# Performance work log

Hardware: AMD Instinct MI355X
Metric: run time of the kernel (lower is better)

Reference implementation:

```python
import jax, jax.numpy as jnp
import numpy as np

S, H, E, DFF = 8192, 1024, 8, 4096
CAPACITY = (S * 1) // E  # capacity_factor=1.0, k=1 -> 1024 (>= min_capacity 4)


def setup_inputs() -> dict:
    key = jax.random.key(0)
    ks = jax.random.split(key, 6)
    sc_in = 1.0 / np.sqrt(H)
    sc_ff = 1.0 / np.sqrt(DFF)
    return {
        "hidden_states": jax.random.normal(ks[0], (S, H), dtype=jnp.float32),
        "wg": jax.random.normal(ks[1], (H, E), dtype=jnp.float32) * sc_in,
        "w1": jax.random.normal(ks[2], (E, H, DFF), dtype=jnp.float32) * sc_in,
        "b1": jnp.zeros((E, DFF), dtype=jnp.float32),
        "w2": jax.random.normal(ks[3], (E, DFF, H), dtype=jnp.float32) * sc_ff,
        "b2": jnp.zeros((E, H), dtype=jnp.float32),
    }


def _top1_gate(x, wg):
    # DeepSpeed top1gating (noisy_gate_policy=None, used_token=None)
    logits = x @ wg                                   # [S, E]
    gates = jax.nn.softmax(logits, axis=-1)           # [S, E]
    idx = jnp.argmax(gates, axis=-1)                  # [S]
    mask1 = jax.nn.one_hot(idx, E, dtype=gates.dtype) # [S, E]
    # load-balancing aux loss (uses pre-capacity mask)
    me = jnp.mean(gates, axis=0)
    ce = jnp.mean(mask1, axis=0)
    l_aux = jnp.sum(me * ce) * E
    # capacity-based token dropping
    locations1 = jnp.cumsum(mask1, axis=0) - 1.0      # position within expert
    mask1 = mask1 * (locations1 < CAPACITY)
    exp_counts = jnp.sum(mask1, axis=0).astype(jnp.int32)
    loc_s = jnp.sum(locations1 * mask1, axis=1).astype(jnp.int32)   # [S]
    loc_sc = jax.nn.one_hot(loc_s, CAPACITY, dtype=gates.dtype)     # [S, C]
    combine = jnp.einsum("se,sc->sec", gates * mask1, loc_sc)       # [S, E, C]
    dispatch = (combine > 0).astype(gates.dtype)
    return l_aux, combine, dispatch, exp_counts


def reference(hidden_states, wg, w1, b1, w2, b2):
    l_aux, combine, dispatch, exp_counts = _top1_gate(hidden_states, wg)
    # dispatch tokens to expert slots: [E, C, H]
    disp = jnp.einsum("sec,sh->ech", dispatch, hidden_states)
    # grouped expert FFN (GELU MLP)
    h1 = jax.nn.gelu(jnp.einsum("ech,ehf->ecf", disp, w1) + b1[:, None, :])
    eo = jnp.einsum("ecf,efh->ech", h1, w2) + b2[:, None, :]
    # combine back to token order, weighted by gate values
    out = jnp.einsum("sec,ech->sh", combine, eo)      # [S, H]
    # dropout prob = 0.0 -> identity
    return out, l_aux, exp_counts
```

## Files before the change

### kernel.cpp

```cpp
#include <hip/hip_runtime.h>

#define S_TOK 8192
#define H_DIM 1024
#define NE    8
#define CAP   1024
#define DFF   4096

typedef unsigned short u16;
typedef __bf16 bf16_t;
typedef bf16_t bf16x8 __attribute__((ext_vector_type(8)));
typedef float  f32x4  __attribute__((ext_vector_type(4)));
typedef unsigned short u16x8 __attribute__((ext_vector_type(8)));

__device__ __forceinline__ u16 f2bf(float f) {
  union { float f; unsigned u; } a; a.f = f;
  unsigned u = a.u;
  u += 0x7fffu + ((u >> 16) & 1u);
  return (u16)(u >> 16);
}

__device__ __forceinline__ float gelu_fast(float x) {
  float u = 1.5957691216057308f * x * (1.0f + 0.044715f * x * x);
  float ez = __expf(-u);
  return x * __builtin_amdgcn_rcpf(1.0f + ez);
}

__global__ __launch_bounds__(256) void gate_kernel(const float* __restrict__ x,
                                                   const float* __restrict__ wg,
                            float* __restrict__ gate, int* __restrict__ expert,
                            int* __restrict__ rank, int* __restrict__ blockCnt,
                            float* __restrict__ blockMe) {
  __shared__ float sg[16][8];
  __shared__ int   se[16];
  int tid = threadIdx.x, lane = tid & 63, w = tid >> 6;
  int b = blockIdx.x;
  int t0 = w * 4;
  const float* xr[4];
#pragma unroll
  for (int t = 0; t < 4; ++t) xr[t] = x + (size_t)(b * 16 + t0 + t) * H_DIM;

  float acc[4][8];
#pragma unroll
  for (int t = 0; t < 4; ++t)
#pragma unroll
    for (int e = 0; e < 8; ++e) acc[t][e] = 0.f;

#pragma unroll
  for (int i = 0; i < 4; ++i) {
    int h = lane * 4 + i * 256;
    float4 xv[4];
#pragma unroll
    for (int t = 0; t < 4; ++t) xv[t] = *(const float4*)(xr[t] + h);
    float4 wrow[8];
#pragma unroll
    for (int k = 0; k < 4; ++k) {
      wrow[2 * k]     = *(const float4*)(wg + (size_t)(h + k) * 8);
      wrow[2 * k + 1] = *(const float4*)(wg + (size_t)(h + k) * 8 + 4);
    }
#pragma unroll
    for (int t = 0; t < 4; ++t) {
      float xs[4] = {xv[t].x, xv[t].y, xv[t].z, xv[t].w};
#pragma unroll
      for (int k = 0; k < 4; ++k) {
        float xx = xs[k];
        float4 wa = wrow[2 * k], wb = wrow[2 * k + 1];
        acc[t][0] += xx * wa.x; acc[t][1] += xx * wa.y;
        acc[t][2] += xx * wa.z; acc[t][3] += xx * wa.w;
        acc[t][4] += xx * wb.x; acc[t][5] += xx * wb.y;
        acc[t][6] += xx * wb.z; acc[t][7] += xx * wb.w;
      }
    }
  }
#pragma unroll
  for (int off = 32; off >= 1; off >>= 1)
#pragma unroll
    for (int t = 0; t < 4; ++t)
#pragma unroll
      for (int e = 0; e < 8; ++e) acc[t][e] += __shfl_down(acc[t][e], off);

  if (lane == 0) {
#pragma unroll
    for (int t = 0; t < 4; ++t) {
      int tt = t0 + t, s = b * 16 + tt;
      float mx = acc[t][0];
#pragma unroll
      for (int e = 1; e < 8; ++e) mx = fmaxf(mx, acc[t][e]);
      float g[8], Z = 0.f;
#pragma unroll
      for (int e = 0; e < 8; ++e) { g[e] = __expf(acc[t][e] - mx); Z += g[e]; }
      int am = 0; float best = acc[t][0];
#pragma unroll
      for (int e = 1; e < 8; ++e) if (acc[t][e] > best) { best = acc[t][e]; am = e; }
      float inv = 1.f / Z;
#pragma unroll
      for (int e = 0; e < 8; ++e) sg[tt][e] = g[e] * inv;
      se[tt] = am;
      gate[s] = g[am] * inv;
      expert[s] = am;
    }
  }
  __syncthreads();
  if (tid < 16) {
    int e = se[tid], r = 0;
    for (int t2 = 0; t2 < tid; ++t2) r += (se[t2] == e) ? 1 : 0;
    rank[b * 16 + tid] = r;
  }
  if (tid < 8) {
    int c = 0; float m = 0.f;
#pragma unroll
    for (int t = 0; t < 16; ++t) { c += (se[t] == tid) ? 1 : 0; m += sg[t][tid]; }
    blockCnt[b * 8 + tid] = c;
    blockMe[b * 8 + tid] = m;
  }
}

__global__ void scan_kernel(const int* __restrict__ blockCnt, const float* __restrict__ blockMe,
                            int* __restrict__ blockOff, int* __restrict__ counts,
                            float* __restrict__ tail) {
  int tid = threadIdx.x;
  int e = tid >> 6, lane = tid & 63;
  int run = 0; float msum = 0.f;
  for (int c = 0; c < 8; ++c) {
    int b = c * 64 + lane;
    int v = blockCnt[b * 8 + e];
    float mv = blockMe[b * 8 + e];
    int sc = v;
#pragma unroll
    for (int off = 1; off < 64; off <<= 1) {
      int u = __shfl_up(sc, off);
      if (lane >= off) sc += u;
    }
    blockOff[b * 8 + e] = run + sc - v;
    run += __shfl(sc, 63);
#pragma unroll
    for (int off = 32; off >= 1; off >>= 1) mv += __shfl_down(mv, off);
    msum += __shfl(mv, 0);
  }
  __shared__ float sm[8];
  __shared__ int scnt[8];
  if (lane == 0) {
    sm[e] = msum; scnt[e] = run;
    counts[e] = run < CAP ? run : CAP;
  }
  __syncthreads();
  if (tid == 0) {
    float la = 0.f;
    for (int i = 0; i < 8; ++i)
      la += (sm[i] / (float)S_TOK) * ((float)scnt[i] / (float)S_TOK);
    tail[0] = la * (float)NE;
    for (int i = 0; i < 8; ++i) {
      int cc = scnt[i] < CAP ? scnt[i] : CAP;
      tail[1 + i] = (float)cc;
    }
  }
}

__global__ void assign_kernel(const int* __restrict__ expert, const int* __restrict__ rank,
                              const int* __restrict__ blockOff, int* __restrict__ slot_token) {
  int s = blockIdx.x * 256 + threadIdx.x;
  int e = expert[s];
  int pos = blockOff[(s >> 4) * 8 + e] + rank[s];
  if (pos < CAP) slot_token[e * CAP + pos] = s;
}

__global__ void gather_kernel(const float* __restrict__ x, const int* __restrict__ slot_token,
                              const int* __restrict__ counts, u16* __restrict__ disp) {
  int slot = blockIdx.x;
  int e = slot >> 10, c = slot & 1023;
  int t = threadIdx.x;
  ushort4 v4;
  if (c < counts[e]) {
    int s = slot_token[slot];
    float4 v = *(const float4*)(x + (size_t)s * H_DIM + t * 4);
    v4.x = f2bf(v.x); v4.y = f2bf(v.y); v4.z = f2bf(v.z); v4.w = f2bf(v.w);
  } else {
    v4.x = 0; v4.y = 0; v4.z = 0; v4.w = 0;
  }
  *(ushort4*)(disp + (size_t)slot * H_DIM + t * 4) = v4;
}

__global__ void transpose_convert(const float* __restrict__ src0, u16* __restrict__ dst0,
                                  int R, int C) {
  __shared__ float tile[64][65];
  int e = blockIdx.z;
  const float* src = src0 + (size_t)e * R * C;
  u16* dst = dst0 + (size_t)e * R * C;
  int c0 = blockIdx.x * 64, r0 = blockIdx.y * 64;
  int g = threadIdx.x & 15, rr = threadIdx.x >> 4;
#pragma unroll
  for (int p = 0; p < 4; ++p) {
    int r = rr + p * 16;
    float4 v = *(const float4*)(src + (size_t)(r0 + r) * C + c0 + g * 4);
    tile[r][g * 4 + 0] = v.x;
    tile[r][g * 4 + 1] = v.y;
    tile[r][g * 4 + 2] = v.z;
    tile[r][g * 4 + 3] = v.w;
  }
  __syncthreads();
  int g2 = threadIdx.x & 7, c2 = threadIdx.x >> 3;
#pragma unroll
  for (int p = 0; p < 2; ++p) {
    int c = c2 + p * 32;
    u16x8 o;
#pragma unroll
    for (int k = 0; k < 8; ++k) o[k] = f2bf(tile[g2 * 8 + k][c]);
    *(u16x8*)(dst + (size_t)(c0 + c) * R + r0 + g2 * 8) = o;
  }
}

__global__ __launch_bounds__(256, 3) void gemm1_kernel(const u16* __restrict__ disp,
                                                       const u16* __restrict__ w1t,
                                                       const float* __restrict__ b1,
                                                       u16* __restrict__ h1) {
  __shared__ __align__(16) u16 As[8192];
  __shared__ __align__(16) u16 Bs[8192];
  int flat = blockIdx.x;
  int swz = (flat & 7) * 256 + (flat >> 3);
  int e  = swz >> 8;
  int r  = swz & 255;
  int bx = r >> 3;
  int by = r & 7;
  int m0 = by * 128, n0 = bx * 128;
  const u16* A  = disp + (size_t)e * CAP * H_DIM + (size_t)m0 * H_DIM;
  const u16* Bt = w1t + (size_t)e * DFF * H_DIM + (size_t)n0 * H_DIM;

  int tid = threadIdx.x, lane = tid & 63, w = tid >> 6;
  int wm = w >> 1, wn = w & 1, q = lane >> 4, l15 = lane & 15;

  const u16* gpA[4]; const u16* gpB[4]; int lofs[4];
#pragma unroll
  for (int i = 0; i < 4; ++i) {
    int p = (w * 4 + i) * 64 + lane;
    int row = p >> 3, slot = p & 7;
    int kq = slot ^ (row & 7);
    gpA[i] = A + (size_t)row * H_DIM + kq * 8;
    gpB[i] = Bt + (size_t)row * H_DIM + kq * 8;
    lofs[i] = (w * 4 + i) * 512;
  }

  int aoff[2][4], boff[2][4];
#pragma unroll
  for (int t = 0; t < 4; ++t) {
    int ra = wm * 64 + t * 16 + l15;
    int rb = wn * 64 + t * 16 + l15;
#pragma unroll
    for (int s = 0; s < 2; ++s) {
      aoff[s][t] = ra * 64 + (((s * 4) + q) ^ (ra & 7)) * 8;
      boff[s][t] = rb * 64 + (((s * 4) + q) ^ (rb & 7)) * 8;
    }
  }

  f32x4 acc[4][4];
  f32x4 zero = {0.f, 0.f, 0.f, 0.f};
#pragma unroll
  for (int i = 0; i < 4; ++i)
#pragma unroll
    for (int j = 0; j < 4; ++j) acc[i][j] = zero;

  for (int kt = 0; kt < H_DIM; kt += 64) {
#pragma unroll
    for (int i = 0; i < 4; ++i) {
      __builtin_amdgcn_global_load_lds((__attribute__((address_space(1))) int*)(gpA[i] + kt),
                                       (__attribute__((address_space(3))) int*)(As + lofs[i]), 16, 0, 0);
      __builtin_amdgcn_global_load_lds((__attribute__((address_space(1))) int*)(gpB[i] + kt),
                                       (__attribute__((address_space(3))) int*)(Bs + lofs[i]), 16, 0, 0);
    }
    __syncthreads();
#pragma unroll
    for (int s = 0; s < 2; ++s) {
      bf16x8 af[4], bfr[4];
#pragma unroll
      for (int t = 0; t < 4; ++t) af[t] = *(const bf16x8*)(As + aoff[s][t]);
#pragma unroll
      for (int t = 0; t < 4; ++t) bfr[t] = *(const bf16x8*)(Bs + boff[s][t]);
#pragma unroll
      for (int mt = 0; mt < 4; ++mt)
#pragma unroll
        for (int nt = 0; nt < 4; ++nt)
          acc[mt][nt] = __builtin_amdgcn_mfma_f32_16x16x32_bf16(af[mt], bfr[nt], acc[mt][nt], 0, 0, 0);
    }
    __syncthreads();
  }

  const float* b1e = b1 + e * DFF;
  u16* out = h1 + (size_t)e * CAP * DFF;
#pragma unroll
  for (int mt = 0; mt < 4; ++mt)
#pragma unroll
    for (int nt = 0; nt < 4; ++nt) {
      int col = n0 + wn * 64 + nt * 16 + l15;
      float bias = b1e[col];
#pragma unroll
      for (int rr = 0; rr < 4; ++rr) {
        int row = m0 + wm * 64 + mt * 16 + q * 4 + rr;
        out[(size_t)row * DFF + col] = f2bf(gelu_fast(acc[mt][nt][rr] + bias));
      }
    }
}

__global__ __launch_bounds__(512, 4) void gemm2_kernel(const u16* __restrict__ h1,
                                                       const u16* __restrict__ w2t,
                                                       const float* __restrict__ b2,
                                                       const int* __restrict__ slot_token,
                                                       const float* __restrict__ gate,
                                                       const int* __restrict__ counts,
                                                       float* __restrict__ out) {
  __shared__ __align__(16) u16 As[8192];
  __shared__ __align__(16) u16 Bs[8192];
  int flat = blockIdx.x;
  int swz = (flat & 7) * 64 + (flat >> 3);
  int e  = swz >> 6;
  int r  = swz & 63;
  int bx = r & 7;
  int by = r >> 3;
  int m0 = by * 128, n0 = bx * 128;
  const u16* A  = h1 + (size_t)e * CAP * DFF + (size_t)m0 * DFF;
  const u16* Bt = w2t + (size_t)e * H_DIM * DFF + (size_t)n0 * DFF;
  int tid = threadIdx.x, lane = tid & 63, w = tid >> 6;
  int wm = w >> 2, wn = w & 3;
  int q = lane >> 4, l15 = lane & 15;
  f32x4 acc[4][2];
  f32x4 zero = {0.f, 0.f, 0.f, 0.f};
#pragma unroll
  for (int i = 0; i < 4; ++i) { acc[i][0] = zero; acc[i][1] = zero; }

  const u16* gsrc = (w < 4) ? A : Bt;
  u16* ldst = (w < 4) ? As : Bs;
  int q4 = w & 3;
  const u16* gp[4]; int lofs[4];
#pragma unroll
  for (int i = 0; i < 4; ++i) {
    int p = (q4 * 4 + i) * 64 + lane;
    int row = p >> 3, slot = p & 7;
    int kq = slot ^ (row & 7);
    gp[i] = gsrc + (size_t)row * DFF + kq * 8;
    lofs[i] = (q4 * 4 + i) * 512;
  }

  int aoff[2][4], boff[2][2];
#pragma unroll
  for (int t = 0; t < 4; ++t) {
    int ra = wm * 64 + t * 16 + l15;
#pragma unroll
    for (int s = 0; s < 2; ++s)
      aoff[s][t] = ra * 64 + (((s * 4) + q) ^ (ra & 7)) * 8;
  }
#pragma unroll
  for (int t = 0; t < 2; ++t) {
    int rb = wn * 32 + t * 16 + l15;
#pragma unroll
    for (int s = 0; s < 2; ++s)
      boff[s][t] = rb * 64 + (((s * 4) + q) ^ (rb & 7)) * 8;
  }

  for (int kt = 0; kt < DFF; kt += 64) {
#pragma unroll
    for (int i = 0; i < 4; ++i)
      __builtin_amdgcn_global_load_lds((__attribute__((address_space(1))) int*)(gp[i] + kt),
                                       (__attribute__((address_space(3))) int*)(ldst + lofs[i]), 16, 0, 0);
    __syncthreads();
#pragma unroll
    for (int s = 0; s < 2; ++s) {
      bf16x8 af[4], bfr[2];
#pragma unroll
      for (int t = 0; t < 4; ++t) af[t] = *(const bf16x8*)(As + aoff[s][t]);
#pragma unroll
      for (int t = 0; t < 2; ++t) bfr[t] = *(const bf16x8*)(Bs + boff[s][t]);
#pragma unroll
      for (int mt = 0; mt < 4; ++mt)
#pragma unroll
        for (int nt = 0; nt < 2; ++nt)
          acc[mt][nt] = __builtin_amdgcn_mfma_f32_16x16x32_bf16(af[mt], bfr[nt], acc[mt][nt], 0, 0, 0);
    }
    __syncthreads();
  }

  int cnt = counts[e];
  const float* b2e = b2 + e * H_DIM;
#pragma unroll
  for (int mt = 0; mt < 4; ++mt) {
    int tok[4]; float gv[4];
#pragma unroll
    for (int rr = 0; rr < 4; ++rr) {
      int c = m0 + wm * 64 + mt * 16 + q * 4 + rr;
      if (c < cnt) { int s = slot_token[e * CAP + c]; tok[rr] = s; gv[rr] = gate[s]; }
      else { tok[rr] = -1; gv[rr] = 0.f; }
    }
#pragma unroll
    for (int nt = 0; nt < 2; ++nt) {
      int col = n0 + wn * 32 + nt * 16 + l15;
      float bias = b2e[col];
#pragma unroll
      for (int rr = 0; rr < 4; ++rr)
        if (tok[rr] >= 0)
          out[(size_t)tok[rr] * H_DIM + col] = gv[rr] * (acc[mt][nt][rr] + bias);
    }
  }
}

extern "C" void kernel_launch(void* const* d_in, const int* in_sizes, int n_in,
                              void* d_out, int out_size, void* d_ws, size_t ws_size,
                              hipStream_t stream) {
  const float* x  = (const float*)d_in[0];
  const float* wg = (const float*)d_in[1];
  const float* w1 = (const float*)d_in[2];
  const float* b1 = (const float*)d_in[3];
  const float* w2 = (const float*)d_in[4];
  const float* b2 = (const float*)d_in[5];
  float* out = (float*)d_out;
  char* ws = (char*)d_ws;
  const size_t MB = 1024 * 1024;
  u16* w1t  = (u16*)(ws);
  u16* w2t  = (u16*)(ws + 64 * MB);
  u16* disp = (u16*)(ws + 128 * MB);
  u16* h1   = (u16*)(ws + 144 * MB);
  char* sm = ws + 208 * MB;
  float* gate      = (float*)(sm);
  int*   expert    = (int*)(sm + 32 * 1024);
  int*   rank      = (int*)(sm + 64 * 1024);
  int*   slot_tok  = (int*)(sm + 96 * 1024);
  int*   blockCnt  = (int*)(sm + 128 * 1024);
  int*   blockOff  = (int*)(sm + 144 * 1024);
  float* blockMe   = (float*)(sm + 160 * 1024);
  int*   counts    = (int*)(sm + 176 * 1024);

  hipMemsetAsync(d_out, 0, (size_t)out_size * sizeof(float), stream);
  gate_kernel<<<512, 256, 0, stream>>>(x, wg, gate, expert, rank, blockCnt, blockMe);
  scan_kernel<<<1, 512, 0, stream>>>(blockCnt, blockMe, blockOff, counts,
                                     out + (size_t)S_TOK * H_DIM);
  assign_kernel<<<32, 256, 0, stream>>>(expert, rank, blockOff, slot_tok);
  gather_kernel<<<8192, 256, 0, stream>>>(x, slot_tok, counts, disp);
  transpose_convert<<<dim3(DFF / 64, H_DIM / 64, NE), 256, 0, stream>>>(w1, w1t, H_DIM, DFF);
  transpose_convert<<<dim3(H_DIM / 64, DFF / 64, NE), 256, 0, stream>>>(w2, w2t, DFF, H_DIM);
  gemm1_kernel<<<2048, 256, 0, stream>>>(disp, w1t, b1, h1);
  gemm2_kernel<<<512, 512, 0, stream>>>(h1, w2t, b2, slot_tok, gate, counts, out);
}
```

Baseline: 547.4 us.

## Double-buffer LDS in both expert GEMMs and merge weight transpose launches

Both grouped GEMMs move from a single 64-wide K tile with two barriers per step to double-buffered 32-wide K tiles. The next tile is fetched with global_load_lds while MFMAs run on the current one, using one barrier per step and a new XOR swizzle for the 32-element rows. The two weight transpose/convert launches are merged into one kernel with 128x64 tiles. The aim is to overlap global-to-LDS loads with compute and cut one launch, at the cost of twice as many loop iterations and more barriers overall.

```diff
diff --git a/kernel.cpp b/kernel.cpp
--- a/kernel.cpp
+++ b/kernel.cpp
@@ -179,16 +179,28 @@
   *(ushort4*)(disp + (size_t)slot * H_DIM + t * 4) = v4;
 }
 
-__global__ void transpose_convert(const float* __restrict__ src0, u16* __restrict__ dst0,
-                                  int R, int C) {
-  __shared__ float tile[64][65];
-  int e = blockIdx.z;
-  const float* src = src0 + (size_t)e * R * C;
-  u16* dst = dst0 + (size_t)e * R * C;
-  int c0 = blockIdx.x * 64, r0 = blockIdx.y * 64;
+__global__ __launch_bounds__(256) void transpose_convert2(const float* __restrict__ w1,
+                                                          u16* __restrict__ w1t,
+                                                          const float* __restrict__ w2,
+                                                          u16* __restrict__ w2t) {
+  __shared__ float tile[128][65];
+  int bid = blockIdx.x;
+  const float* src; u16* dst; int R, C, r0, c0;
+  if (bid < 4096) {
+    int e = bid >> 9, t = bid & 511;
+    R = H_DIM; C = DFF;
+    src = w1 + (size_t)e * R * C; dst = w1t + (size_t)e * R * C;
+    r0 = (t & 7) * 128; c0 = (t >> 3) * 64;
+  } else {
+    int b2 = bid - 4096;
+    int e = b2 >> 9, t = b2 & 511;
+    R = DFF; C = H_DIM;
+    src = w2 + (size_t)e * R * C; dst = w2t + (size_t)e * R * C;
+    r0 = (t & 31) * 128; c0 = (t >> 5) * 64;
+  }
   int g = threadIdx.x & 15, rr = threadIdx.x >> 4;
 #pragma unroll
-  for (int p = 0; p < 4; ++p) {
+  for (int p = 0; p < 8; ++p) {
     int r = rr + p * 16;
     float4 v = *(const float4*)(src + (size_t)(r0 + r) * C + c0 + g * 4);
     tile[r][g * 4 + 0] = v.x;
@@ -197,10 +209,10 @@
     tile[r][g * 4 + 3] = v.w;
   }
   __syncthreads();
-  int g2 = threadIdx.x & 7, c2 = threadIdx.x >> 3;
-#pragma unroll
-  for (int p = 0; p < 2; ++p) {
-    int c = c2 + p * 32;
+  int g2 = threadIdx.x & 15, c2 = threadIdx.x >> 4;
+#pragma unroll
+  for (int p = 0; p < 4; ++p) {
+    int c = c2 + p * 16;
     u16x8 o;
 #pragma unroll
     for (int k = 0; k < 8; ++k) o[k] = f2bf(tile[g2 * 8 + k][c]);
@@ -212,8 +224,8 @@
                                                        const u16* __restrict__ w1t,
                                                        const float* __restrict__ b1,
                                                        u16* __restrict__ h1) {
-  __shared__ __align__(16) u16 As[8192];
-  __shared__ __align__(16) u16 Bs[8192];
+  __shared__ __align__(16) u16 As[2][4096];
+  __shared__ __align__(16) u16 Bs[2][4096];
   int flat = blockIdx.x;
   int swz = (flat & 7) * 256 + (flat >> 3);
   int e  = swz >> 8;
@@ -227,27 +239,24 @@
   int tid = threadIdx.x, lane = tid & 63, w = tid >> 6;
   int wm = w >> 1, wn = w & 1, q = lane >> 4, l15 = lane & 15;
 
-  const u16* gpA[4]; const u16* gpB[4]; int lofs[4];
-#pragma unroll
-  for (int i = 0; i < 4; ++i) {
-    int p = (w * 4 + i) * 64 + lane;
-    int row = p >> 3, slot = p & 7;
-    int kq = slot ^ (row & 7);
+  const u16* gpA[2]; const u16* gpB[2]; int lofs[2];
+#pragma unroll
+  for (int i = 0; i < 2; ++i) {
+    int p = (w * 2 + i) * 64 + lane;
+    int row = p >> 2;
+    int kq = (p & 3) ^ ((row >> 1) & 3);
     gpA[i] = A + (size_t)row * H_DIM + kq * 8;
     gpB[i] = Bt + (size_t)row * H_DIM + kq * 8;
-    lofs[i] = (w * 4 + i) * 512;
-  }
-
-  int aoff[2][4], boff[2][4];
+    lofs[i] = (w * 2 + i) * 512;
+  }
+
+  int aoff[4], boff[4];
 #pragma unroll
   for (int t = 0; t < 4; ++t) {
     int ra = wm * 64 + t * 16 + l15;
+    aoff[t] = ra * 32 + ((q ^ ((ra >> 1) & 3)) * 8);
     int rb = wn * 64 + t * 16 + l15;
-#pragma unroll
-    for (int s = 0; s < 2; ++s) {
-      aoff[s][t] = ra * 64 + (((s * 4) + q) ^ (ra & 7)) * 8;
-      boff[s][t] = rb * 64 + (((s * 4) + q) ^ (rb & 7)) * 8;
-    }
+    boff[t] = rb * 32 + ((q ^ ((rb >> 1) & 3)) * 8);
   }
 
   f32x4 acc[4][4];
@@ -257,29 +266,39 @@
 #pragma unroll
     for (int j = 0; j < 4; ++j) acc[i][j] = zero;
 
-  for (int kt = 0; kt < H_DIM; kt += 64) {
-#pragma unroll
-    for (int i = 0; i < 4; ++i) {
-      __builtin_amdgcn_global_load_lds((__attribute__((address_space(1))) int*)(gpA[i] + kt),
-                                       (__attribute__((address_space(3))) int*)(As + lofs[i]), 16, 0, 0);
-      __builtin_amdgcn_global_load_lds((__attribute__((address_space(1))) int*)(gpB[i] + kt),
-                                       (__attribute__((address_space(3))) int*)(Bs + lofs[i]), 16, 0, 0);
-    }
+#pragma unroll
+  for (int i = 0; i < 2; ++i) {
+    __builtin_amdgcn_global_load_lds((__attribute__((address_space(1))) int*)(gpA[i]),
+                                     (__attribute__((address_space(3))) int*)(&As[0][0] + lofs[i]), 16, 0, 0);
+    __builtin_amdgcn_global_load_lds((__attribute__((address_space(1))) int*)(gpB[i]),
+                                     (__attribute__((address_space(3))) int*)(&Bs[0][0] + lofs[i]), 16, 0, 0);
+  }
+  __syncthreads();
+
+  int cur = 0;
+  for (int kt = 0; kt < H_DIM; kt += 32) {
+    if (kt + 32 < H_DIM) {
+      int nxt = cur ^ 1;
+#pragma unroll
+      for (int i = 0; i < 2; ++i) {
+        __builtin_amdgcn_global_load_lds((__attribute__((address_space(1))) int*)(gpA[i] + kt + 32),
+                                         (__attribute__((address_space(3))) int*)(&As[nxt][0] + lofs[i]), 16, 0, 0);
+        __builtin_amdgcn_global_load_lds((__attribute__((address_space(1))) int*)(gpB[i] + kt + 32),
+                                         (__attribute__((address_space(3))) int*)(&Bs[nxt][0] + lofs[i]), 16, 0, 0);
+      }
+    }
+    bf16x8 af[4], bfr[4];
+#pragma unroll
+    for (int t = 0; t < 4; ++t) af[t] = *(const bf16x8*)(&As[cur][0] + aoff[t]);
+#pragma unroll
+    for (int t = 0; t < 4; ++t) bfr[t] = *(const bf16x8*)(&Bs[cur][0] + boff[t]);
+#pragma unroll
+    for (int mt = 0; mt < 4; ++mt)
+#pragma unroll
+      for (int nt = 0; nt < 4; ++nt)
+        acc[mt][nt] = __builtin_amdgcn_mfma_f32_16x16x32_bf16(af[mt], bfr[nt], acc[mt][nt], 0, 0, 0);
     __syncthreads();
-#pragma unroll
-    for (int s = 0; s < 2; ++s) {
-      bf16x8 af[4], bfr[4];
-#pragma unroll
-      for (int t = 0; t < 4; ++t) af[t] = *(const bf16x8*)(As + aoff[s][t]);
-#pragma unroll
-      for (int t = 0; t < 4; ++t) bfr[t] = *(const bf16x8*)(Bs + boff[s][t]);
-#pragma unroll
-      for (int mt = 0; mt < 4; ++mt)
-#pragma unroll
-        for (int nt = 0; nt < 4; ++nt)
-          acc[mt][nt] = __builtin_amdgcn_mfma_f32_16x16x32_bf16(af[mt], bfr[nt], acc[mt][nt], 0, 0, 0);
-    }
-    __syncthreads();
+    cur ^= 1;
   }
 
   const float* b1e = b1 + e * DFF;
@@ -305,8 +324,8 @@
                                                        const float* __restrict__ gate,
                                                        const int* __restrict__ counts,
                                                        float* __restrict__ out) {
-  __shared__ __align__(16) u16 As[8192];
-  __shared__ __align__(16) u16 Bs[8192];
+  __shared__ __align__(16) u16 As[2][4096];
+  __shared__ __align__(16) u16 Bs[2][4096];
   int flat = blockIdx.x;
   int swz = (flat & 7) * 64 + (flat >> 3);
   int e  = swz >> 6;
@@ -325,54 +344,61 @@
   for (int i = 0; i < 4; ++i) { acc[i][0] = zero; acc[i][1] = zero; }
 
   const u16* gsrc = (w < 4) ? A : Bt;
-  u16* ldst = (w < 4) ? As : Bs;
+  int isA = (w < 4) ? 1 : 0;
   int q4 = w & 3;
-  const u16* gp[4]; int lofs[4];
-#pragma unroll
-  for (int i = 0; i < 4; ++i) {
-    int p = (q4 * 4 + i) * 64 + lane;
-    int row = p >> 3, slot = p & 7;
-    int kq = slot ^ (row & 7);
+  const u16* gp[2]; int lofs[2];
+#pragma unroll
+  for (int i = 0; i < 2; ++i) {
+    int p = (q4 * 2 + i) * 64 + lane;
+    int row = p >> 2;
+    int kq = (p & 3) ^ ((row >> 1) & 3);
     gp[i] = gsrc + (size_t)row * DFF + kq * 8;
-    lofs[i] = (q4 * 4 + i) * 512;
-  }
-
-  int aoff[2][4], boff[2][2];
+    lofs[i] = (q4 * 2 + i) * 512;
+  }
+
+  int aoff[4], boff[2];
 #pragma unroll
   for (int t = 0; t < 4; ++t) {
     int ra = wm * 64 + t * 16 + l15;
-#pragma unroll
-    for (int s = 0; s < 2; ++s)
-      aoff[s][t] = ra * 64 + (((s * 4) + q) ^ (ra & 7)) * 8;
+    aoff[t] = ra * 32 + ((q ^ ((ra >> 1) & 3)) * 8);
   }
 #pragma unroll
   for (int t = 0; t < 2; ++t) {
     int rb = wn * 32 + t * 16 + l15;
-#pragma unroll
-    for (int s = 0; s < 2; ++s)
-      boff[s][t] = rb * 64 + (((s * 4) + q) ^ (rb & 7)) * 8;
-  }
-
-  for (int kt = 0; kt < DFF; kt += 64) {
-#pragma unroll
-    for (int i = 0; i < 4; ++i)
-      __builtin_amdgcn_global_load_lds((__attribute__((address_space(1))) int*)(gp[i] + kt),
-                                       (__attribute__((address_space(3))) int*)(ldst + lofs[i]), 16, 0, 0);
+    boff[t] = rb * 32 + ((q ^ ((rb >> 1) & 3)) * 8);
+  }
+
+  {
+    u16* sb = isA ? &As[0][0] : &Bs[0][0];
+#pragma unroll
+    for (int i = 0; i < 2; ++i)
+      __builtin_amdgcn_global_load_lds((__attribute__((address_space(1))) int*)(gp[i]),
+                                       (__attribute__((address_space(3))) int*)(sb + lofs[i]), 16, 0, 0);
+  }
+  __syncthreads();
+
+  int cur = 0;
+  for (int kt = 0; kt < DFF; kt += 32) {
+    if (kt + 32 < DFF) {
+      int nxt = cur ^ 1;
+      u16* sb = isA ? &As[nxt][0] : &Bs[nxt][0];
+#pragma unroll
+      for (int i = 0; i < 2; ++i)
+        __builtin_amdgcn_global_load_lds((__attribute__((address_space(1))) int*)(gp[i] + kt + 32),
+                                         (__attribute__((address_space(3))) int*)(sb + lofs[i]), 16, 0, 0);
+    }
+    bf16x8 af[4], bfr[2];
+#pragma unroll
+    for (int t = 0; t < 4; ++t) af[t] = *(const bf16x8*)(&As[cur][0] + aoff[t]);
+#pragma unroll
+    for (int t = 0; t < 2; ++t) bfr[t] = *(const bf16x8*)(&Bs[cur][0] + boff[t]);
+#pragma unroll
+    for (int mt = 0; mt < 4; ++mt)
+#pragma unroll
+      for (int nt = 0; nt < 2; ++nt)
+        acc[mt][nt] = __builtin_amdgcn_mfma_f32_16x16x32_bf16(af[mt], bfr[nt], acc[mt][nt], 0, 0, 0);
     __syncthreads();
-#pragma unroll
-    for (int s = 0; s < 2; ++s) {
-      bf16x8 af[4], bfr[2];
-#pragma unroll
-      for (int t = 0; t < 4; ++t) af[t] = *(const bf16x8*)(As + aoff[s][t]);
-#pragma unroll
-      for (int t = 0; t < 2; ++t) bfr[t] = *(const bf16x8*)(Bs + boff[s][t]);
-#pragma unroll
-      for (int mt = 0; mt < 4; ++mt)
-#pragma unroll
-        for (int nt = 0; nt < 2; ++nt)
-          acc[mt][nt] = __builtin_amdgcn_mfma_f32_16x16x32_bf16(af[mt], bfr[nt], acc[mt][nt], 0, 0, 0);
-    }
-    __syncthreads();
+    cur ^= 1;
   }
 
   int cnt = counts[e];
@@ -430,8 +456,7 @@
                                      out + (size_t)S_TOK * H_DIM);
   assign_kernel<<<32, 256, 0, stream>>>(expert, rank, blockOff, slot_tok);
   gather_kernel<<<8192, 256, 0, stream>>>(x, slot_tok, counts, disp);
-  transpose_convert<<<dim3(DFF / 64, H_DIM / 64, NE), 256, 0, stream>>>(w1, w1t, H_DIM, DFF);
-  transpose_convert<<<dim3(H_DIM / 64, DFF / 64, NE), 256, 0, stream>>>(w2, w2t, DFF, H_DIM);
+  transpose_convert2<<<8192, 256, 0, stream>>>(w1, w1t, w2, w2t);
   gemm1_kernel<<<2048, 256, 0, stream>>>(disp, w1t, b1, h1);
   gemm2_kernel<<<512, 512, 0, stream>>>(h1, w2t, b2, slot_tok, gate, counts, out);
 }
```

Result: no change. 558.0 us (+1.9%).
